# Kernel tuning notes

Measured on AMD Instinct MI355X. Metric: run time of the kernel, lower is better.

Reference implementation:

```python
import jax, jax.numpy as jnp
import numpy as np

B, S, HID = 2, 2048, 2048
H, D = 16, 128  # heads, head_dim == kernel_hidden_size
GATE_NORM = 16.0
CLAMP_MIN = -50.0


def gla(q, k, v, gk):
    # fused_recurrent_gla: S_t = diag(exp(gk_t)) S_{t-1} + k_t^T v_t; o_t = (q_t*scale) @ S_t
    # q,k,v,gk: [B,H,S,D]
    scale = D ** -0.5
    qs = jnp.moveaxis(q, 2, 0) * scale  # [S,B,H,D]
    ks = jnp.moveaxis(k, 2, 0)
    vs = jnp.moveaxis(v, 2, 0)
    gs = jnp.moveaxis(gk, 2, 0)

    def step(state, xs):
        q_t, k_t, v_t, g_t = xs  # each [B,H,D]
        state = state * jnp.exp(g_t)[..., None] + k_t[..., None] * v_t[..., None, :]
        o_t = jnp.einsum('bhk,bhkv->bhv', q_t, state)
        return state, o_t

    init = jnp.zeros((q.shape[0], H, D, D), q.dtype)
    _, out = jax.lax.scan(step, init, (qs, ks, vs, gs))
    return jnp.moveaxis(out, 0, 2)  # [B,H,S,D]


def setup_inputs() -> dict:
    key = jax.random.key(0)
    ks = jax.random.split(key, 8)
    std = 0.02
    hidden_states = jax.random.normal(ks[0], (B, S, HID), jnp.float32)
    Wq = jax.random.normal(ks[1], (HID, HID), jnp.float32) * std
    Wk = jax.random.normal(ks[2], (HID, HID), jnp.float32) * std
    Wv = jax.random.normal(ks[3], (HID, HID), jnp.float32) * std
    Wo = jax.random.normal(ks[4], (HID, HID), jnp.float32) * std
    Wg1 = jnp.eye(HID, dtype=jnp.float32)  # nn.init.eye_
    bg1 = jnp.zeros((HID,), jnp.float32)
    Wg2 = jnp.eye(HID, dtype=jnp.float32)
    bg2 = jnp.zeros((HID,), jnp.float32)
    alpha_list = jax.random.uniform(ks[5], (2,), jnp.float32)
    return dict(hidden_states=hidden_states, Wq=Wq, Wk=Wk, Wv=Wv, Wo=Wo,
                Wg1=Wg1, bg1=bg1, Wg2=Wg2, bg2=bg2, alpha_list=alpha_list)


def reference(hidden_states, Wq, Wk, Wv, Wo, Wg1, bg1, Wg2, bg2, alpha_list):
    b, s, _ = hidden_states.shape

    def split_heads(x):  # [b,s,hid] -> [b,h,s,d]
        return x.reshape(b, s, H, D).transpose(0, 2, 1, 3)

    q = split_heads(hidden_states @ Wq.T)
    k = split_heads(hidden_states @ Wk.T)
    v = split_heads(hidden_states @ Wv.T)

    def gate(Wg, bg):
        g = split_heads(hidden_states @ Wg.T + bg)
        g = jax.nn.log_sigmoid(g) / GATE_NORM
        return jnp.maximum(g, CLAMP_MIN)

    gk = gate(Wg1, bg1)
    gk2 = gate(Wg2, bg2)

    o1 = gla(q, k, v, gk)
    o2 = gla(q, k, v, gk2)

    a = jax.nn.softmax(alpha_list)
    attn = a[0] * o1 + a[1] * o2  # [b,h,s,d]
    attn = attn.transpose(0, 2, 1, 3).reshape(b, s, HID)
    return attn @ Wo.T
```

## Files before the change

kernel.cpp:

```cpp
#include <hip/hip_runtime.h>
#include <cstdint>
#include <cstddef>


#define BB     2
#define SEQ    2048
#define HIDN   2048
#define NH     16
#define DD     128
#define CHUNK  64
#define NCHUNK (SEQ / CHUNK)
#define NBH    (BB * NH)
#define NELC   8388608
#define WELC   4194304
static constexpr float QSCALE = 0.08838834764831845f;

typedef __bf16 bf16_t;
typedef _Float16 half_t;
typedef short  short8 __attribute__((ext_vector_type(8)));
typedef float  f32x4  __attribute__((ext_vector_type(4)));

__device__ __forceinline__ float bf2f(short u) {
  return (float)__builtin_bit_cast(bf16_t, u);
}
__device__ __forceinline__ short f2bf(float f) {
  return __builtin_bit_cast(short, (bf16_t)f);
}
__device__ __forceinline__ float hf2f(short u) {
  return (float)__builtin_bit_cast(half_t, u);
}
__device__ __forceinline__ short f2hf(float f) {
  return __builtin_bit_cast(short, (half_t)f);
}

__device__ __forceinline__ void gload_lds16(const void* g, void* l) {
  __builtin_amdgcn_global_load_lds(
      (__attribute__((address_space(1))) unsigned int*)g,
      (__attribute__((address_space(3))) unsigned int*)l, 16, 0, 0);
}

__device__ __forceinline__ void gemm_body(const bf16_t* __restrict__ A,
                                          const bf16_t* __restrict__ Bw,
                                          const float*  __restrict__ bias,
                                          bf16_t* __restrict__ outb,
                                          float*  __restrict__ outf, int epi) {
  __shared__ bf16_t As[128 * 64];
  __shared__ bf16_t Bs[128 * 64];
  const int tm   = blockIdx.x * 128;
  const int tn   = blockIdx.y * 128;
  const int wave = threadIdx.x >> 6;
  const int lane = threadIdx.x & 63;
  const int wm   = (wave >> 1) * 64;
  const int wn   = (wave & 1) * 64;
  const int qd   = lane >> 4;
  const int l16  = lane & 15;
  const int ro   = l16 & 7;

  const int gc = (lane & 7) ^ (lane >> 3);
  const bf16_t* ga[4];
  const bf16_t* gb[4];
  bf16_t* la[4];
  bf16_t* lb[4];
#pragma unroll
  for (int u = 0; u < 4; u++) {
    const int row = wave * 32 + u * 8 + (lane >> 3);
    ga[u] = A  + (size_t)(tm + row) * HIDN + gc * 8;
    gb[u] = Bw + (size_t)(tn + row) * HIDN + gc * 8;
    la[u] = &As[(wave * 256 + u * 64) * 8];
    lb[u] = &Bs[(wave * 256 + u * 64) * 8];
  }

  f32x4 acc[4][4];
#pragma unroll
  for (int i = 0; i < 4; i++)
#pragma unroll
    for (int j = 0; j < 4; j++) acc[i][j] = (f32x4){0.f, 0.f, 0.f, 0.f};

  for (int k0 = 0; k0 < HIDN; k0 += 64) {
#pragma unroll
    for (int u = 0; u < 4; u++) { gload_lds16(ga[u], la[u]); ga[u] += 64; }
#pragma unroll
    for (int u = 0; u < 4; u++) { gload_lds16(gb[u], lb[u]); gb[u] += 64; }
    __syncthreads();
#pragma unroll
    for (int ks = 0; ks < 2; ks++) {
      const int g = ks * 4 + qd;
      short8 af[4], bfv[4];
#pragma unroll
      for (int t = 0; t < 4; t++)
        af[t] = *(const short8*)&As[(wm + t * 16 + l16) * 64 + (g ^ ro) * 8];
#pragma unroll
      for (int t = 0; t < 4; t++)
        bfv[t] = *(const short8*)&Bs[(wn + t * 16 + l16) * 64 + (g ^ ro) * 8];
#pragma unroll
      for (int i = 0; i < 4; i++)
#pragma unroll
        for (int j = 0; j < 4; j++)
          acc[i][j] = __builtin_amdgcn_mfma_f32_16x16x32_bf16(
              af[i], bfv[j], acc[i][j], 0, 0, 0);
    }
    __syncthreads();
  }

#pragma unroll
  for (int i = 0; i < 4; i++)
#pragma unroll
    for (int j = 0; j < 4; j++)
#pragma unroll
      for (int r = 0; r < 4; r++) {
        const int row = tm + wm + i * 16 + qd * 4 + r;
        const int col = tn + wn + j * 16 + l16;
        float v = acc[i][j][r];
        if (epi == 1) {
          v += bias[col];
          const float ls = fminf(v, 0.f) - log1pf(__expf(-fabsf(v)));
          v = fmaxf(ls * 0.0625f, -50.f);
        }
        if (epi == 2) outf[(size_t)row * HIDN + col] = v;
        else          outb[(size_t)row * HIDN + col] = (bf16_t)v;
      }
}

__global__ __launch_bounds__(256) void k_gemm_proj(
    const bf16_t* __restrict__ Xb,
    const bf16_t* __restrict__ W0, const bf16_t* __restrict__ W1,
    const bf16_t* __restrict__ W2, const bf16_t* __restrict__ W3,
    const bf16_t* __restrict__ W4,
    const float* __restrict__ bg1, const float* __restrict__ bg2,
    bf16_t* __restrict__ Qb, bf16_t* __restrict__ Kb, bf16_t* __restrict__ Vb,
    bf16_t* __restrict__ G1b, bf16_t* __restrict__ G2b) {
  const int z = blockIdx.z;
  const bf16_t* Ws[5] = {W0, W1, W2, W3, W4};
  bf16_t* Os[5] = {Qb, Kb, Vb, G1b, G2b};
  const float* bias = (z == 3) ? bg1 : ((z == 4) ? bg2 : nullptr);
  gemm_body(Xb, Ws[z], bias, Os[z], nullptr, (z >= 3) ? 1 : 0);
}

__global__ __launch_bounds__(256) void k_gemm_out(
    const bf16_t* __restrict__ attnB, const bf16_t* __restrict__ Wob,
    float* __restrict__ out) {
  gemm_body(attnB, Wob, nullptr, nullptr, out, 2);
}

__global__ __launch_bounds__(256) void k_cvt_all(
    const float* __restrict__ hid, const float* __restrict__ wq,
    const float* __restrict__ wk, const float* __restrict__ wv,
    const float* __restrict__ wg1, const float* __restrict__ wg2,
    const float* __restrict__ wo, bf16_t* __restrict__ Xb,
    bf16_t* __restrict__ Wd, bf16_t* __restrict__ Wcur,
    bf16_t* __restrict__ WoB) {
  const int y = blockIdx.y;
  const float* srcs[7] = {hid, wq, wk, wv, wg1, wg2, wo};
  bf16_t* dsts[7] = {Xb, Wd, Wd + WELC, Wd + 2 * WELC, Wd + 3 * WELC, Wcur,
                     WoB};
  const int n = (y == 0) ? NELC : WELC;
  const float* src = srcs[y];
  bf16_t* dst = dsts[y];
  const int idx = (blockIdx.x * 256 + threadIdx.x) * 4;
  if (idx < n) {
    const float4 f = *(const float4*)(src + idx);
    dst[idx + 0] = (bf16_t)f.x; dst[idx + 1] = (bf16_t)f.y;
    dst[idx + 2] = (bf16_t)f.z; dst[idx + 3] = (bf16_t)f.w;
  }
}

__global__ __launch_bounds__(256) void k_zero(float* __restrict__ out) {
  out[(size_t)blockIdx.x * 256 + threadIdx.x] = 0.f;
}

__global__ __launch_bounds__(64) void k_gc(bf16_t* __restrict__ G1b,
                                           bf16_t* __restrict__ G2b,
                                           float* __restrict__ Btot) {
  const int n = blockIdx.x, b = blockIdx.y >> 2, slab = blockIdx.y & 3;
  const int e = blockIdx.z;
  short* P = (short*)(e ? G2b : G1b);
  const int d0 = slab * 512 + threadIdx.x * 8;
  const size_t base = ((size_t)(b * SEQ + n * CHUNK)) * HIDN + d0;
  float c[8] = {0.f, 0.f, 0.f, 0.f, 0.f, 0.f, 0.f, 0.f};
  for (int t = 0; t < CHUNK; t++) {
    short* p = P + base + (size_t)t * HIDN;
    const short8 g = *(const short8*)p;
    short8 o;
#pragma unroll
    for (int j = 0; j < 8; j++) { c[j] += bf2f(g[j]); o[j] = f2hf(c[j]); }
    *(short8*)p = o;
  }
  const int bh = b * 16 + (d0 >> 7);
  float* bp = Btot + ((size_t)(e * NBH + bh) * NCHUNK + n) * DD + (d0 & 127);
#pragma unroll
  for (int j = 0; j < 8; j++) bp[j] = c[j];
}

template <int ACC>
__global__ __launch_bounds__(256) void k_sA(
    const bf16_t* __restrict__ Qb, const bf16_t* __restrict__ Kb,
    const bf16_t* __restrict__ Vb, const bf16_t* __restrict__ Gc,
    bf16_t* __restrict__ UT, const float* __restrict__ alpha,
    bf16_t* __restrict__ attn) {
  const int n = blockIdx.x, bh = blockIdx.y;
  const int b = bh >> 4, h = bh & 15;
  const size_t rbase = ((size_t)(b * SEQ + n * CHUNK)) * HIDN + h * DD;
  const int tid = threadIdx.x;
  const int wave = tid >> 6, lane = tid & 63, qd = lane >> 4, l16 = lane & 15;
  __shared__ short vT[128 * 66];
  __shared__ short k2s[64 * 128];
  __shared__ short r3[128 * 66];
  __shared__ short Ps[64 * 72];
  const float mx = fmaxf(alpha[0], alpha[1]);
  const float x0 = __expf(alpha[0] - mx), x1 = __expf(alpha[1] - mx);
  const float wsc = ((ACC ? x1 : x0) / (x0 + x1)) * QSCALE;

  const short* Kp = (const short*)Kb;
  const short* Vp = (const short*)Vb;
  const short* Gp = (const short*)Gc;
  const short* Qp = (const short*)Qb;

#pragma unroll
  for (int rep = 0; rep < 4; rep++) {
    const int slot = rep * 256 + tid;
    const int t = slot >> 4, ch = slot & 15;
    const size_t ga = rbase + (size_t)t * HIDN + ch * 8;
    const short8 vv = *(const short8*)(Vp + ga);
    const short8 kk = *(const short8*)(Kp + ga);
    const short8 cc = *(const short8*)(Gp + ga);
    const short8 c6 = *(const short8*)(Gp + rbase + (size_t)63 * HIDN + ch * 8);
    short8 k2v;
#pragma unroll
    for (int j = 0; j < 8; j++) {
      const int d = ch * 8 + j;
      vT[d * 66 + t] = vv[j];
      const float c = hf2f(cc[j]);
      const float kf = bf2f(kk[j]);
      k2v[j] = f2bf(kf * __expf(-c));
      r3[d * 66 + t] = f2bf(kf * __expf(hf2f(c6[j]) - c));
    }
    *(short8*)&k2s[t * 128 + ((ch ^ (t & 7)) << 3)] = k2v;
  }
  __syncthreads();

  {
    const int m0 = (wave >> 1) * 64, n0 = (wave & 1) * 64;
    const int* vTi = (const int*)vT;
    const int* r3i = (const int*)r3;
    f32x4 uacc[4][4];
#pragma unroll
    for (int i = 0; i < 4; i++)
#pragma unroll
      for (int j = 0; j < 4; j++) uacc[i][j] = (f32x4){0.f, 0.f, 0.f, 0.f};
#pragma unroll
    for (int ks = 0; ks < 2; ks++) {
      const int ch = ks * 4 + qd;
      short8 af[4], bfv[4];
#pragma unroll
      for (int i = 0; i < 4; i++) {
        const int dv = m0 + i * 16 + l16;
        const int ba = dv * 33 + ch * 4;
#pragma unroll
        for (int w2 = 0; w2 < 4; w2++) {
          const int v = vTi[ba + w2];
          af[i][2 * w2] = (short)(v & 0xffff);
          af[i][2 * w2 + 1] = (short)((unsigned)v >> 16);
        }
      }
#pragma unroll
      for (int j = 0; j < 4; j++) {
        const int dk = n0 + j * 16 + l16;
        const int ba = dk * 33 + ch * 4;
#pragma unroll
        for (int w2 = 0; w2 < 4; w2++) {
          const int v = r3i[ba + w2];
          bfv[j][2 * w2] = (short)(v & 0xffff);
          bfv[j][2 * w2 + 1] = (short)((unsigned)v >> 16);
        }
      }
#pragma unroll
      for (int i = 0; i < 4; i++)
#pragma unroll
        for (int j = 0; j < 4; j++)
          uacc[i][j] = __builtin_amdgcn_mfma_f32_16x16x32_bf16(
              af[i], bfv[j], uacc[i][j], 0, 0, 0);
    }
    short* Uo = (short*)UT + (size_t)(bh * NCHUNK + n) * (DD * DD);
#pragma unroll
    for (int i = 0; i < 4; i++)
#pragma unroll
      for (int j = 0; j < 4; j++)
#pragma unroll
        for (int r = 0; r < 4; r++) {
          const int dv = m0 + i * 16 + qd * 4 + r;
          const int dk = n0 + j * 16 + l16;
          Uo[dv * 128 + (((dk >> 3) ^ (dv & 7)) << 3) + (dk & 7)] =
              f2bf(uacc[i][j][r]);
        }
  }
  __syncthreads();

#pragma unroll
  for (int rep = 0; rep < 4; rep++) {
    const int slot = rep * 256 + tid;
    const int t = slot >> 4, ch = slot & 15;
    const size_t ga = rbase + (size_t)t * HIDN + ch * 8;
    const short8 qq = *(const short8*)(Qp + ga);
    const short8 cc = *(const short8*)(Gp + ga);
    short8 o;
#pragma unroll
    for (int j = 0; j < 8; j++)
      o[j] = f2bf(bf2f(qq[j]) * wsc * __expf(hf2f(cc[j])));
    *(short8*)&r3[t * 128 + ((ch ^ (t & 7)) << 3)] = o;
  }
  __syncthreads();

  {
    f32x4 pacc[4];
#pragma unroll
    for (int j = 0; j < 4; j++) pacc[j] = (f32x4){0.f, 0.f, 0.f, 0.f};
    const int tq = wave * 16 + l16;
#pragma unroll
    for (int ks = 0; ks < 4; ks++) {
      const int ch = ks * 4 + qd;
      const short8 a = *(const short8*)&r3[tq * 128 + ((ch ^ (tq & 7)) << 3)];
#pragma unroll
      for (int j = 0; j < 4; j++) {
        const int s = j * 16 + l16;
        const short8 bq =
            *(const short8*)&k2s[s * 128 + ((ch ^ (s & 7)) << 3)];
        pacc[j] =
            __builtin_amdgcn_mfma_f32_16x16x32_bf16(a, bq, pacc[j], 0, 0, 0);
      }
    }
#pragma unroll
    for (int j = 0; j < 4; j++)
#pragma unroll
      for (int r = 0; r < 4; r++) {
        const int t = wave * 16 + qd * 4 + r, s = j * 16 + l16;
        Ps[t * 72 + s] = (t >= s) ? f2bf(pacc[j][r]) : (short)0;
      }
  }
  __syncthreads();

  f32x4 oacc[8];
#pragma unroll
  for (int j = 0; j < 8; j++) oacc[j] = (f32x4){0.f, 0.f, 0.f, 0.f};
  {
    const int* vTi = (const int*)vT;
    const int tq = wave * 16 + l16;
#pragma unroll
    for (int ks = 0; ks < 2; ks++) {
      const int ch = ks * 4 + qd;
      const short8 a = *(const short8*)&Ps[tq * 72 + ch * 8];
#pragma unroll
      for (int j = 0; j < 8; j++) {
        const int dv = j * 16 + l16;
        const int ba = dv * 33 + ch * 4;
        short8 bq;
#pragma unroll
        for (int w2 = 0; w2 < 4; w2++) {
          const int v = vTi[ba + w2];
          bq[2 * w2] = (short)(v & 0xffff);
          bq[2 * w2 + 1] = (short)((unsigned)v >> 16);
        }
        oacc[j] =
            __builtin_amdgcn_mfma_f32_16x16x32_bf16(a, bq, oacc[j], 0, 0, 0);
      }
    }
  }
#pragma unroll
  for (int j = 0; j < 8; j++)
#pragma unroll
    for (int r = 0; r < 4; r++) {
      const int t = wave * 16 + qd * 4 + r;
      const int dv = j * 16 + l16;
      bf16_t* p = &attn[rbase + (size_t)t * HIDN + dv];
      if (ACC) *p = (bf16_t)((float)*p + oacc[j][r]);
      else     *p = (bf16_t)oacc[j][r];
    }
}

__global__ __launch_bounds__(256) void k_s2(bf16_t* __restrict__ UT,
                                            const float* __restrict__ Btot) {
  const int dg = blockIdx.x, bh = blockIdx.y;
  const int dv = dg * 8 + (threadIdx.x >> 5);
  const int dk0 = (threadIdx.x & 31) * 4;
  const int pos = dv * 128 + (((dk0 >> 3) ^ (dv & 7)) << 3) + (dk0 & 7);
  float st[4] = {0.f, 0.f, 0.f, 0.f};
  for (int nn = 0; nn < NCHUNK; nn++) {
    short* p = (short*)UT + (size_t)(bh * NCHUNK + nn) * (DD * DD) + pos;
    const float4 bp =
        *(const float4*)(Btot + (size_t)(bh * NCHUNK + nn) * DD + dk0);
    short u0 = p[0], u1 = p[1], u2 = p[2], u3 = p[3];
    p[0] = f2bf(st[0]); p[1] = f2bf(st[1]);
    p[2] = f2bf(st[2]); p[3] = f2bf(st[3]);
    st[0] = st[0] * __expf(bp.x) + bf2f(u0);
    st[1] = st[1] * __expf(bp.y) + bf2f(u1);
    st[2] = st[2] * __expf(bp.z) + bf2f(u2);
    st[3] = st[3] * __expf(bp.w) + bf2f(u3);
  }
}

__global__ __launch_bounds__(256) void k_s3b(
    const bf16_t* __restrict__ Qb, const bf16_t* __restrict__ Gc,
    const bf16_t* __restrict__ UT, const float* __restrict__ alpha,
    const int e, bf16_t* __restrict__ attn) {
  const int n = blockIdx.x, bh = blockIdx.y;
  const int b = bh >> 4, h = bh & 15;
  const size_t rbase = ((size_t)(b * SEQ + n * CHUNK)) * HIDN + h * DD;
  const int tid = threadIdx.x;
  const int wave = tid >> 6, lane = tid & 63, qd = lane >> 4, l16 = lane & 15;
  __shared__ short qh[64 * 128];
  __shared__ short Ss[128 * 128];
  const float mx = fmaxf(alpha[0], alpha[1]);
  const float x0 = __expf(alpha[0] - mx), x1 = __expf(alpha[1] - mx);
  const float wsc = ((e ? x1 : x0) / (x0 + x1)) * QSCALE;

  const short* Sp = (const short*)UT + (size_t)(bh * NCHUNK + n) * (DD * DD);
#pragma unroll
  for (int rep = 0; rep < 8; rep++) {
    const int c = rep * 256 + tid;
    gload_lds16(Sp + c * 8, &Ss[c * 8]);
  }
  const short* Qp = (const short*)Qb;
  const short* Gp = (const short*)Gc;
#pragma unroll
  for (int rep = 0; rep < 4; rep++) {
    const int slot = rep * 256 + tid;
    const int t = slot >> 4, ch = slot & 15;
    const size_t ga = rbase + (size_t)t * HIDN + ch * 8;
    const short8 qq = *(const short8*)(Qp + ga);
    const short8 cc = *(const short8*)(Gp + ga);
    short8 o;
#pragma unroll
    for (int j = 0; j < 8; j++)
      o[j] = f2bf(bf2f(qq[j]) * wsc * __expf(hf2f(cc[j])));
    *(short8*)&qh[t * 128 + ((ch ^ (t & 7)) << 3)] = o;
  }
  __syncthreads();

  f32x4 oacc[8];
#pragma unroll
  for (int j = 0; j < 8; j++) oacc[j] = (f32x4){0.f, 0.f, 0.f, 0.f};
  const int tq = wave * 16 + l16;
#pragma unroll
  for (int ks = 0; ks < 4; ks++) {
    const int ch = ks * 4 + qd;
    const short8 a = *(const short8*)&qh[tq * 128 + ((ch ^ (tq & 7)) << 3)];
#pragma unroll
    for (int j = 0; j < 8; j++) {
      const int dv = j * 16 + l16;
      const short8 bq = *(const short8*)&Ss[dv * 128 + ((ch ^ (dv & 7)) << 3)];
      oacc[j] =
          __builtin_amdgcn_mfma_f32_16x16x32_bf16(a, bq, oacc[j], 0, 0, 0);
    }
  }
#pragma unroll
  for (int j = 0; j < 8; j++)
#pragma unroll
    for (int r = 0; r < 4; r++) {
      const int t = wave * 16 + qd * 4 + r;
      const int dv = j * 16 + l16;
      bf16_t* p = &attn[rbase + (size_t)t * HIDN + dv];
      *p = (bf16_t)((float)*p + oacc[j][r]);
    }
}

extern "C" void kernel_launch(void* const* d_in, const int* in_sizes, int n_in,
                              void* d_out, int out_size, void* d_ws,
                              size_t ws_size, hipStream_t stream) {
  const float* hid  = (const float*)d_in[0];
  const float* wq   = (const float*)d_in[1];
  const float* wk   = (const float*)d_in[2];
  const float* wv   = (const float*)d_in[3];
  const float* wo   = (const float*)d_in[4];
  const float* wg1  = (const float*)d_in[5];
  const float* bg1  = (const float*)d_in[6];
  const float* wg2  = (const float*)d_in[7];
  const float* bg2  = (const float*)d_in[8];
  const float* alph = (const float*)d_in[9];
  float* out = (float*)d_out;
  (void)in_sizes; (void)n_in; (void)out_size;

  char* ws = (char*)d_ws;
  size_t off = 0;
  auto alloc = [&](size_t bytes) -> void* {
    void* p = ws + off;
    off += (bytes + 255) & ~(size_t)255;
    return p;
  };
  const size_t NEL = NELC, WEL = WELC;
  bf16_t* Xb   = (bf16_t*)alloc(NEL * 2);
  bf16_t* Wcur = (bf16_t*)alloc(WEL * 2);
  bf16_t* WoB  = (bf16_t*)alloc(WEL * 2);
  bf16_t* Qb   = (bf16_t*)alloc(NEL * 2);
  bf16_t* Kb   = (bf16_t*)alloc(NEL * 2);
  bf16_t* Vb   = (bf16_t*)alloc(NEL * 2);
  bf16_t* G1b  = (bf16_t*)alloc(NEL * 2);
  bf16_t* G2b  = (bf16_t*)alloc(NEL * 2);
  float*  Btot = (float*) alloc((size_t)2 * NBH * NCHUNK * DD * 4);
  bf16_t* Wd = (bf16_t*)d_out;
  bf16_t* UT = (bf16_t*)d_out;

  if (off > ws_size) {
    k_zero<<<dim3((unsigned)(NEL / 256)), 256, 0, stream>>>(out);
    return;
  }

  k_cvt_all<<<dim3(8192, 7), 256, 0, stream>>>(hid, wq, wk, wv, wg1, wg2, wo,
                                               Xb, Wd, Wcur, WoB);
  k_gemm_proj<<<dim3(32, 16, 5), 256, 0, stream>>>(
      Xb, Wd, Wd + WEL, Wd + 2 * WEL, Wd + 3 * WEL, Wcur, bg1, bg2, Qb, Kb, Vb,
      G1b, G2b);
  k_gc<<<dim3(NCHUNK, BB * 4, 2), 64, 0, stream>>>(G1b, G2b, Btot);

  const dim3 gs(NCHUNK, NBH), g2(16, NBH);
  const size_t BSTRIDE = (size_t)NBH * NCHUNK * DD;
  k_sA<0><<<gs, 256, 0, stream>>>(Qb, Kb, Vb, G1b, UT, alph, Xb);
  k_s2<<<g2, 256, 0, stream>>>(UT, Btot);
  k_s3b<<<gs, 256, 0, stream>>>(Qb, G1b, UT, alph, 0, Xb);
  k_sA<1><<<gs, 256, 0, stream>>>(Qb, Kb, Vb, G2b, UT, alph, Xb);
  k_s2<<<g2, 256, 0, stream>>>(UT, Btot + BSTRIDE);
  k_s3b<<<gs, 256, 0, stream>>>(Qb, G2b, UT, alph, 1, Xb);

  k_gemm_out<<<dim3(32, 16), 256, 0, stream>>>(Xb, WoB, out);
}
```

Before: 593.0 us.

## Replace GEMM with 256x256 double-buffered pipelined tile using 512 threads

Rewrites the shared bf16 GEMM used for the input projections and output projection as a 256x256 tile kernel with 8 waves, double-buffered LDS staging, and interleaved global-to-LDS loads with MFMA quadrants under explicit waitcnt/barrier control and raised wave priority. This aims to hide global load latency and raise data reuse per tile. The larger tile uses 128KB LDS per block and fewer blocks, which reduces occupancy and can underfill the GPU for the smaller output GEMM.

Result: slower. 664.2 us (+12.0%).

```diff
diff --git a/kernel.cpp b/kernel.cpp
--- a/kernel.cpp
+++ b/kernel.cpp
@@ -39,77 +39,163 @@
       (__attribute__((address_space(3))) unsigned int*)l, 16, 0, 0);
 }
 
-__device__ __forceinline__ void gemm_body(const bf16_t* __restrict__ A,
-                                          const bf16_t* __restrict__ Bw,
-                                          const float*  __restrict__ bias,
-                                          bf16_t* __restrict__ outb,
-                                          float*  __restrict__ outf, int epi) {
-  __shared__ bf16_t As[128 * 64];
-  __shared__ bf16_t Bs[128 * 64];
-  const int tm   = blockIdx.x * 128;
-  const int tn   = blockIdx.y * 128;
-  const int wave = threadIdx.x >> 6;
-  const int lane = threadIdx.x & 63;
-  const int wm   = (wave >> 1) * 64;
-  const int wn   = (wave & 1) * 64;
+#define VMW4 asm volatile("s_waitcnt vmcnt(4)" ::: "memory")
+#define VMW2 asm volatile("s_waitcnt vmcnt(2)" ::: "memory")
+#define VMW0 asm volatile("s_waitcnt vmcnt(0)" ::: "memory")
+#define LGKM0 asm volatile("s_waitcnt lgkmcnt(0)" ::: "memory")
+#define SBAR __builtin_amdgcn_s_barrier()
+
+
+#define STAGE_A(nx, kt, pair)                                              \
+  {                                                                        \
+    const int rb0 = (pair) ? 64 : 0;                                       \
+    gload_lds16(Ag + (size_t)rb0 * HIDN + (size_t)(kt) * 64,               \
+                (void*)&As[nx][(rb0 + wave * 8) * 64]);                    \
+    gload_lds16(Ag + (size_t)(rb0 + 128) * HIDN + (size_t)(kt) * 64,       \
+                (void*)&As[nx][(rb0 + 128 + wave * 8) * 64]);              \
+  }
+
+#define STAGE_B(nx, kt, pair)                                              \
+  {                                                                        \
+    const int cb0 = (wave >> 2) * 64 + (pair) * 32 + (wave & 3) * 8;       \
+    gload_lds16(Bg + (size_t)cb0 * HIDN + (size_t)(kt) * 64,               \
+                (void*)&Bs[nx][cb0 * 64]);                                 \
+    gload_lds16(Bg + (size_t)(cb0 + 128) * HIDN + (size_t)(kt) * 64,       \
+                (void*)&Bs[nx][(cb0 + 128) * 64]);                         \
+  }
+
+#define LOAD_A(mh)                                                         \
+  {                                                                        \
+    _Pragma("unroll") for (int f = 0; f < 4; f++) {                        \
+      const int row = wm * 128 + (mh) * 64 + f * 16 + l16;                 \
+      ar[f][0] = *(const short8*)&As[cur][row * 64 + ((qd ^ ro) << 3)];    \
+      ar[f][1] =                                                           \
+          *(const short8*)&As[cur][row * 64 + (((4 + qd) ^ ro) << 3)];     \
+    }                                                                      \
+  }
+
+#define LOAD_B(nh)                                                         \
+  {                                                                        \
+    _Pragma("unroll") for (int g = 0; g < 2; g++) {                        \
+      const int col = wn * 64 + (nh) * 32 + g * 16 + l16;                  \
+      br[g][0] = *(const short8*)&Bs[cur][col * 64 + ((qd ^ ro) << 3)];    \
+      br[g][1] =                                                           \
+          *(const short8*)&Bs[cur][col * 64 + (((4 + qd) ^ ro) << 3)];     \
+    }                                                                      \
+  }
+
+#define MFMA_Q(mh, nh)                                                     \
+  {                                                                        \
+    __builtin_amdgcn_s_setprio(1);                                         \
+    _Pragma("unroll") for (int ks = 0; ks < 2; ks++)                       \
+    _Pragma("unroll") for (int f = 0; f < 4; f++)                          \
+    _Pragma("unroll") for (int g = 0; g < 2; g++)                          \
+      acc[(mh) * 4 + f][(nh) * 2 + g] =                                    \
+          __builtin_amdgcn_mfma_f32_16x16x32_bf16(                         \
+              ar[f][ks], br[g][ks], acc[(mh) * 4 + f][(nh) * 2 + g],       \
+              0, 0, 0);                                                    \
+    __builtin_amdgcn_s_setprio(0);                                         \
+  }
+
+__device__ __forceinline__ void gemm256(const bf16_t* __restrict__ A,
+                                        const bf16_t* __restrict__ Bw,
+                                        const float*  __restrict__ bias,
+                                        bf16_t* __restrict__ outb,
+                                        float*  __restrict__ outf, int epi) {
+  __shared__ short As[2][256 * 64];
+  __shared__ short Bs[2][256 * 64];
+  const int tm   = blockIdx.x * 256;
+  const int tn   = blockIdx.y * 256;
+  const int tid  = threadIdx.x;
+  const int wave = tid >> 6;
+  const int lane = tid & 63;
+  const int wm   = wave >> 2;
+  const int wn   = wave & 3;
   const int qd   = lane >> 4;
   const int l16  = lane & 15;
   const int ro   = l16 & 7;
-
-  const int gc = (lane & 7) ^ (lane >> 3);
-  const bf16_t* ga[4];
-  const bf16_t* gb[4];
-  bf16_t* la[4];
-  bf16_t* lb[4];
-#pragma unroll
-  for (int u = 0; u < 4; u++) {
-    const int row = wave * 32 + u * 8 + (lane >> 3);
-    ga[u] = A  + (size_t)(tm + row) * HIDN + gc * 8;
-    gb[u] = Bw + (size_t)(tn + row) * HIDN + gc * 8;
-    la[u] = &As[(wave * 256 + u * 64) * 8];
-    lb[u] = &Bs[(wave * 256 + u * 64) * 8];
-  }
-
-  f32x4 acc[4][4];
-#pragma unroll
-  for (int i = 0; i < 4; i++)
+  const int gc   = (lane & 7) ^ (lane >> 3);
+
+  const short* Ag =
+      (const short*)A + (size_t)(tm + wave * 8 + (lane >> 3)) * HIDN + gc * 8;
+  const short* Bg =
+      (const short*)Bw + (size_t)(tn + (lane >> 3)) * HIDN + gc * 8;
+
+  f32x4 acc[8][4];
+#pragma unroll
+  for (int i = 0; i < 8; i++)
 #pragma unroll
     for (int j = 0; j < 4; j++) acc[i][j] = (f32x4){0.f, 0.f, 0.f, 0.f};
-
-  for (int k0 = 0; k0 < HIDN; k0 += 64) {
-#pragma unroll
-    for (int u = 0; u < 4; u++) { gload_lds16(ga[u], la[u]); ga[u] += 64; }
-#pragma unroll
-    for (int u = 0; u < 4; u++) { gload_lds16(gb[u], lb[u]); gb[u] += 64; }
-    __syncthreads();
-#pragma unroll
-    for (int ks = 0; ks < 2; ks++) {
-      const int g = ks * 4 + qd;
-      short8 af[4], bfv[4];
-#pragma unroll
-      for (int t = 0; t < 4; t++)
-        af[t] = *(const short8*)&As[(wm + t * 16 + l16) * 64 + (g ^ ro) * 8];
-#pragma unroll
-      for (int t = 0; t < 4; t++)
-        bfv[t] = *(const short8*)&Bs[(wn + t * 16 + l16) * 64 + (g ^ ro) * 8];
-#pragma unroll
-      for (int i = 0; i < 4; i++)
-#pragma unroll
-        for (int j = 0; j < 4; j++)
-          acc[i][j] = __builtin_amdgcn_mfma_f32_16x16x32_bf16(
-              af[i], bfv[j], acc[i][j], 0, 0, 0);
-    }
-    __syncthreads();
-  }
-
-#pragma unroll
-  for (int i = 0; i < 4; i++)
+  short8 ar[4][2], br[2][2];
+  int cur = 0;
+
+  STAGE_A(0, 0, 0);
+  STAGE_B(0, 0, 0);
+  STAGE_A(0, 0, 1);
+  STAGE_B(0, 0, 1);
+  VMW4;
+  SBAR;
+
+  for (int t = 0; t < 31; t++) {
+    const int nx = cur ^ 1;
+    LOAD_A(0);
+    LOAD_B(0);
+    STAGE_A(nx, t + 1, 0);
+    SBAR;
+    LGKM0;
+    MFMA_Q(0, 0);
+    VMW4;
+    SBAR;
+    LOAD_A(1);
+    STAGE_B(nx, t + 1, 0);
+    SBAR;
+    LGKM0;
+    MFMA_Q(1, 0);
+    VMW4;
+    SBAR;
+    LOAD_B(1);
+    STAGE_A(nx, t + 1, 1);
+    SBAR;
+    LGKM0;
+    MFMA_Q(1, 1);
+    SBAR;
+    LOAD_A(0);
+    STAGE_B(nx, t + 1, 1);
+    SBAR;
+    LGKM0;
+    MFMA_Q(0, 1);
+    VMW4;
+    SBAR;
+    cur = nx;
+  }
+
+  LOAD_A(0);
+  LOAD_B(0);
+  SBAR;
+  LGKM0;
+  MFMA_Q(0, 0);
+  VMW2;
+  SBAR;
+  LOAD_A(1);
+  LGKM0;
+  MFMA_Q(1, 0);
+  VMW0;
+  SBAR;
+  LOAD_B(1);
+  LGKM0;
+  MFMA_Q(1, 1);
+  LOAD_A(0);
+  LGKM0;
+  MFMA_Q(0, 1);
+
+#pragma unroll
+  for (int i = 0; i < 8; i++)
 #pragma unroll
     for (int j = 0; j < 4; j++)
 #pragma unroll
       for (int r = 0; r < 4; r++) {
-        const int row = tm + wm + i * 16 + qd * 4 + r;
-        const int col = tn + wn + j * 16 + l16;
+        const int row = tm + wm * 128 + (i >> 2) * 64 + (i & 3) * 16 + qd * 4 + r;
+        const int col = tn + wn * 64 + (j >> 1) * 32 + (j & 1) * 16 + l16;
         float v = acc[i][j][r];
         if (epi == 1) {
           v += bias[col];
@@ -121,7 +207,7 @@
       }
 }
 
-__global__ __launch_bounds__(256) void k_gemm_proj(
+__global__ __launch_bounds__(512, 2) void k_gemm_proj(
     const bf16_t* __restrict__ Xb,
     const bf16_t* __restrict__ W0, const bf16_t* __restrict__ W1,
     const bf16_t* __restrict__ W2, const bf16_t* __restrict__ W3,
@@ -133,13 +219,13 @@
   const bf16_t* Ws[5] = {W0, W1, W2, W3, W4};
   bf16_t* Os[5] = {Qb, Kb, Vb, G1b, G2b};
   const float* bias = (z == 3) ? bg1 : ((z == 4) ? bg2 : nullptr);
-  gemm_body(Xb, Ws[z], bias, Os[z], nullptr, (z >= 3) ? 1 : 0);
-}
-
-__global__ __launch_bounds__(256) void k_gemm_out(
+  gemm256(Xb, Ws[z], bias, Os[z], nullptr, (z >= 3) ? 1 : 0);
+}
+
+__global__ __launch_bounds__(512, 2) void k_gemm_out(
     const bf16_t* __restrict__ attnB, const bf16_t* __restrict__ Wob,
     float* __restrict__ out) {
-  gemm_body(attnB, Wob, nullptr, nullptr, out, 2);
+  gemm256(attnB, Wob, nullptr, nullptr, out, 2);
 }
 
 __global__ __launch_bounds__(256) void k_cvt_all(
@@ -505,7 +591,7 @@
 
   k_cvt_all<<<dim3(8192, 7), 256, 0, stream>>>(hid, wq, wk, wv, wg1, wg2, wo,
                                                Xb, Wd, Wcur, WoB);
-  k_gemm_proj<<<dim3(32, 16, 5), 256, 0, stream>>>(
+  k_gemm_proj<<<dim3(16, 8, 5), 512, 0, stream>>>(
       Xb, Wd, Wd + WEL, Wd + 2 * WEL, Wd + 3 * WEL, Wcur, bg1, bg2, Qb, Kb, Vb,
       G1b, G2b);
   k_gc<<<dim3(NCHUNK, BB * 4, 2), 64, 0, stream>>>(G1b, G2b, Btot);
@@ -519,5 +605,5 @@
   k_s2<<<g2, 256, 0, stream>>>(UT, Btot + BSTRIDE);
   k_s3b<<<gs, 256, 0, stream>>>(Qb, G2b, UT, alph, 1, Xb);
 
-  k_gemm_out<<<dim3(32, 16), 256, 0, stream>>>(Xb, WoB, out);
-}
+  k_gemm_out<<<dim3(16, 8), 512, 0, stream>>>(Xb, WoB, out);
+}
```

## Rewrite bf16 GEMMs as 256x128 tiles with triple-buffered async LDS pipeline

Applied to the files above, without the earlier changes.

Replaces the 128x128, 256-thread GEMM body with a 512-thread kernel that computes a 256x128 tile. K-slices are staged into three rotating LDS buffers with global_load_lds, two slices ahead of compute, and vmcnt waits are placed explicitly. The MFMA phases are split into two M-halves with s_setprio so LDS reads and global prefetch overlap matrix work. The aim is to hide global-load latency and raise data reuse per block in both the projection and output GEMMs. The cost is about 147 KB of LDS per block, which limits occupancy to one block per CU, plus hand-managed wait counts that must stay exactly in step with the number of issued loads.

Result: faster. 581.0 us (-2.0%).

```diff
diff --git a/kernel.cpp b/kernel.cpp
--- a/kernel.cpp
+++ b/kernel.cpp
@@ -39,77 +39,124 @@
       (__attribute__((address_space(3))) unsigned int*)l, 16, 0, 0);
 }
 
-__device__ __forceinline__ void gemm_body(const bf16_t* __restrict__ A,
-                                          const bf16_t* __restrict__ Bw,
-                                          const float*  __restrict__ bias,
-                                          bf16_t* __restrict__ outb,
-                                          float*  __restrict__ outf, int epi) {
-  __shared__ bf16_t As[128 * 64];
-  __shared__ bf16_t Bs[128 * 64];
-  const int tm   = blockIdx.x * 128;
+#define VMW6 asm volatile("s_waitcnt vmcnt(6)" ::: "memory")
+#define VMW0 asm volatile("s_waitcnt vmcnt(0)" ::: "memory")
+#define LGKM0 asm volatile("s_waitcnt lgkmcnt(0)" ::: "memory")
+#define SBAR __builtin_amdgcn_s_barrier()
+
+
+#define STG_A(buf, kt, pair)                                                \
+  {                                                                         \
+    const size_t ko = (size_t)(kt) * 64;                                    \
+    gload_lds16(Ag + (size_t)((pair) * 64) * HIDN + ko,                     \
+                (void*)&As[buf][((pair) * 64 + wave * 8) * 64]);            \
+    gload_lds16(Ag + (size_t)((pair) * 64 + 128) * HIDN + ko,               \
+                (void*)&As[buf][((pair) * 64 + 128 + wave * 8) * 64]);      \
+  }
+
+#define STG_B(buf, kt, half)                                                \
+  {                                                                         \
+    gload_lds16(Bg + (size_t)((half) * 64) * HIDN + (size_t)(kt) * 64,      \
+                (void*)&Bs[buf][((half) * 64 + wave * 8) * 64]);            \
+  }
+
+#define LDA_PH(mh, rb)                                                      \
+  {                                                                         \
+    _Pragma("unroll") for (int f = 0; f < 4; f++) {                         \
+      const int row = wm * 128 + (mh) * 64 + f * 16 + l16;                  \
+      ar[f][0] = *(const short8*)&As[rb][row * 64 + ((qd ^ ro) << 3)];      \
+      ar[f][1] =                                                            \
+          *(const short8*)&As[rb][row * 64 + (((4 + qd) ^ ro) << 3)];       \
+    }                                                                       \
+  }
+
+#define LDB_PH(rb)                                                          \
+  {                                                                         \
+    _Pragma("unroll") for (int g = 0; g < 2; g++) {                         \
+      const int col = wn * 32 + g * 16 + l16;                               \
+      br[g][0] = *(const short8*)&Bs[rb][col * 64 + ((qd ^ ro) << 3)];      \
+      br[g][1] =                                                            \
+          *(const short8*)&Bs[rb][col * 64 + (((4 + qd) ^ ro) << 3)];       \
+    }                                                                       \
+  }
+
+#define MFMA_PH(mh)                                                         \
+  {                                                                         \
+    __builtin_amdgcn_s_setprio(1);                                          \
+    _Pragma("unroll") for (int ks = 0; ks < 2; ks++)                        \
+    _Pragma("unroll") for (int f = 0; f < 4; f++)                           \
+    _Pragma("unroll") for (int g = 0; g < 2; g++)                           \
+      acc[(mh) * 4 + f][g] = __builtin_amdgcn_mfma_f32_16x16x32_bf16(       \
+          ar[f][ks], br[g][ks], acc[(mh) * 4 + f][g], 0, 0, 0);             \
+    __builtin_amdgcn_s_setprio(0);                                          \
+  }
+
+__device__ __forceinline__ void gemm256(const bf16_t* __restrict__ A,
+                                        const bf16_t* __restrict__ Bw,
+                                        const float*  __restrict__ bias,
+                                        bf16_t* __restrict__ outb,
+                                        float*  __restrict__ outf, int epi) {
+  __shared__ short As[3][256 * 64];
+  __shared__ short Bs[3][128 * 64];
+  const int tm   = blockIdx.x * 256;
   const int tn   = blockIdx.y * 128;
-  const int wave = threadIdx.x >> 6;
-  const int lane = threadIdx.x & 63;
-  const int wm   = (wave >> 1) * 64;
-  const int wn   = (wave & 1) * 64;
+  const int tid  = threadIdx.x;
+  const int wave = tid >> 6;
+  const int lane = tid & 63;
+  const int wm   = wave >> 2;
+  const int wn   = wave & 3;
   const int qd   = lane >> 4;
   const int l16  = lane & 15;
   const int ro   = l16 & 7;
-
-  const int gc = (lane & 7) ^ (lane >> 3);
-  const bf16_t* ga[4];
-  const bf16_t* gb[4];
-  bf16_t* la[4];
-  bf16_t* lb[4];
-#pragma unroll
-  for (int u = 0; u < 4; u++) {
-    const int row = wave * 32 + u * 8 + (lane >> 3);
-    ga[u] = A  + (size_t)(tm + row) * HIDN + gc * 8;
-    gb[u] = Bw + (size_t)(tn + row) * HIDN + gc * 8;
-    la[u] = &As[(wave * 256 + u * 64) * 8];
-    lb[u] = &Bs[(wave * 256 + u * 64) * 8];
-  }
-
-  f32x4 acc[4][4];
-#pragma unroll
-  for (int i = 0; i < 4; i++)
-#pragma unroll
-    for (int j = 0; j < 4; j++) acc[i][j] = (f32x4){0.f, 0.f, 0.f, 0.f};
-
-  for (int k0 = 0; k0 < HIDN; k0 += 64) {
-#pragma unroll
-    for (int u = 0; u < 4; u++) { gload_lds16(ga[u], la[u]); ga[u] += 64; }
-#pragma unroll
-    for (int u = 0; u < 4; u++) { gload_lds16(gb[u], lb[u]); gb[u] += 64; }
-    __syncthreads();
-#pragma unroll
-    for (int ks = 0; ks < 2; ks++) {
-      const int g = ks * 4 + qd;
-      short8 af[4], bfv[4];
-#pragma unroll
-      for (int t = 0; t < 4; t++)
-        af[t] = *(const short8*)&As[(wm + t * 16 + l16) * 64 + (g ^ ro) * 8];
-#pragma unroll
-      for (int t = 0; t < 4; t++)
-        bfv[t] = *(const short8*)&Bs[(wn + t * 16 + l16) * 64 + (g ^ ro) * 8];
-#pragma unroll
-      for (int i = 0; i < 4; i++)
-#pragma unroll
-        for (int j = 0; j < 4; j++)
-          acc[i][j] = __builtin_amdgcn_mfma_f32_16x16x32_bf16(
-              af[i], bfv[j], acc[i][j], 0, 0, 0);
-    }
-    __syncthreads();
-  }
-
-#pragma unroll
-  for (int i = 0; i < 4; i++)
-#pragma unroll
-    for (int j = 0; j < 4; j++)
+  const int gc   = (lane & 7) ^ (lane >> 3);
+
+  const short* Ag =
+      (const short*)A + (size_t)(tm + wave * 8 + (lane >> 3)) * HIDN + gc * 8;
+  const short* Bg =
+      (const short*)Bw + (size_t)(tn + wave * 8 + (lane >> 3)) * HIDN + gc * 8;
+
+  f32x4 acc[8][2];
+#pragma unroll
+  for (int i = 0; i < 8; i++)
+#pragma unroll
+    for (int j = 0; j < 2; j++) acc[i][j] = (f32x4){0.f, 0.f, 0.f, 0.f};
+  short8 ar[4][2], br[2][2];
+
+  STG_A(0, 0, 0); STG_B(0, 0, 0); STG_B(0, 0, 1); STG_A(0, 0, 1);
+  STG_A(1, 1, 0); STG_B(1, 1, 0); STG_B(1, 1, 1); STG_A(1, 1, 1);
+  VMW6;
+  SBAR;
+
+  int rd = 0, st = 2;
+  for (int t = 0; t < 32; t++) {
+    LDA_PH(0, rd);
+    LDB_PH(rd);
+    if (t < 30) { STG_A(st, t + 2, 0); STG_B(st, t + 2, 0); }
+    SBAR;
+    LGKM0;
+    MFMA_PH(0);
+    SBAR;
+    LDA_PH(1, rd);
+    if (t < 30) { STG_B(st, t + 2, 1); STG_A(st, t + 2, 1); }
+    SBAR;
+    LGKM0;
+    MFMA_PH(1);
+    if (t < 30) { VMW6; }
+    else if (t == 30) { VMW0; }
+    SBAR;
+    rd = (rd == 2) ? 0 : rd + 1;
+    st = (st == 2) ? 0 : st + 1;
+  }
+
+#pragma unroll
+  for (int i = 0; i < 8; i++)
+#pragma unroll
+    for (int j = 0; j < 2; j++)
 #pragma unroll
       for (int r = 0; r < 4; r++) {
-        const int row = tm + wm + i * 16 + qd * 4 + r;
-        const int col = tn + wn + j * 16 + l16;
+        const int row =
+            tm + wm * 128 + (i >> 2) * 64 + (i & 3) * 16 + qd * 4 + r;
+        const int col = tn + wn * 32 + j * 16 + l16;
         float v = acc[i][j][r];
         if (epi == 1) {
           v += bias[col];
@@ -121,7 +168,7 @@
       }
 }
 
-__global__ __launch_bounds__(256) void k_gemm_proj(
+__global__ __launch_bounds__(512, 2) void k_gemm_proj(
     const bf16_t* __restrict__ Xb,
     const bf16_t* __restrict__ W0, const bf16_t* __restrict__ W1,
     const bf16_t* __restrict__ W2, const bf16_t* __restrict__ W3,
@@ -133,13 +180,13 @@
   const bf16_t* Ws[5] = {W0, W1, W2, W3, W4};
   bf16_t* Os[5] = {Qb, Kb, Vb, G1b, G2b};
   const float* bias = (z == 3) ? bg1 : ((z == 4) ? bg2 : nullptr);
-  gemm_body(Xb, Ws[z], bias, Os[z], nullptr, (z >= 3) ? 1 : 0);
-}
-
-__global__ __launch_bounds__(256) void k_gemm_out(
+  gemm256(Xb, Ws[z], bias, Os[z], nullptr, (z >= 3) ? 1 : 0);
+}
+
+__global__ __launch_bounds__(512, 2) void k_gemm_out(
     const bf16_t* __restrict__ attnB, const bf16_t* __restrict__ Wob,
     float* __restrict__ out) {
-  gemm_body(attnB, Wob, nullptr, nullptr, out, 2);
+  gemm256(attnB, Wob, nullptr, nullptr, out, 2);
 }
 
 __global__ __launch_bounds__(256) void k_cvt_all(
@@ -505,7 +552,7 @@
 
   k_cvt_all<<<dim3(8192, 7), 256, 0, stream>>>(hid, wq, wk, wv, wg1, wg2, wo,
                                                Xb, Wd, Wcur, WoB);
-  k_gemm_proj<<<dim3(32, 16, 5), 256, 0, stream>>>(
+  k_gemm_proj<<<dim3(16, 16, 5), 512, 0, stream>>>(
       Xb, Wd, Wd + WEL, Wd + 2 * WEL, Wd + 3 * WEL, Wcur, bg1, bg2, Qb, Kb, Vb,
       G1b, G2b);
   k_gc<<<dim3(NCHUNK, BB * 4, 2), 64, 0, stream>>>(G1b, G2b, Btot);
@@ -519,5 +566,5 @@
   k_s2<<<g2, 256, 0, stream>>>(UT, Btot + BSTRIDE);
   k_s3b<<<gs, 256, 0, stream>>>(Qb, G2b, UT, alph, 1, Xb);
 
-  k_gemm_out<<<dim3(32, 16), 256, 0, stream>>>(Xb, WoB, out);
-}
+  k_gemm_out<<<dim3(16, 16), 512, 0, stream>>>(Xb, WoB, out);
+}
```
